# Kernel optimization log

Measured on AMD Instinct MI355X. Metric: run time of the kernel, lower is better.

The kernel has to match this reference:

```python
import jax, jax.numpy as jnp
import numpy as np

N, G, D, H, B = 32768, 1024, 512, 768, 4   # nodes, graphs, hidden, shared, branches
GHD, NHD = 64, 3                           # graph head dim, node head dim (var_output=1)

def setup_inputs() -> dict:
    key = jax.random.key(0)
    ks = jax.random.split(key, 8)
    scale = 0.02
    x = jax.random.normal(ks[0], (N, D), dtype=jnp.float32)
    batch = jnp.sort(jax.random.randint(ks[1], (N,), 0, G, dtype=jnp.int32))
    dataset_name = jax.random.randint(ks[2], (G,), 0, B, dtype=jnp.int32)
    return {
        "x": x,
        "batch": batch,
        "dataset_name": dataset_name,
        "Wg_shared": jax.random.normal(ks[3], (B, D, H), jnp.float32) * scale,
        "bg_shared": jnp.zeros((B, H), jnp.float32),
        "Wg_head": jax.random.normal(ks[4], (B, H, 2 * GHD), jnp.float32) * scale,
        "bg_head": jnp.zeros((B, 2 * GHD), jnp.float32),
        "Wn1": jax.random.normal(ks[5], (B, D, D), jnp.float32) * scale,
        "bn1": jnp.zeros((B, D), jnp.float32),
        "Wn2": jax.random.normal(ks[6], (B, D, 2 * NHD), jnp.float32) * scale,
        "bn2": jnp.zeros((B, 2 * NHD), jnp.float32),
    }

def _select_branch(y, branch_ids):
    # y: [n, B, f], branch_ids: [n] -> [n, f]
    return jnp.take_along_axis(y, branch_ids[:, None, None], axis=1)[:, 0]

def reference(x, batch, dataset_name, Wg_shared, bg_shared, Wg_head, bg_head,
              Wn1, bn1, Wn2, bn2):
    nG = dataset_name.shape[0]
    # --- graph mean pooling (graph_pool_fn with reduction='mean') ---
    counts = jax.ops.segment_sum(jnp.ones((x.shape[0], 1), x.dtype), batch,
                                 num_segments=nG)
    x_graph = jax.ops.segment_sum(x, batch, num_segments=nG) / jnp.maximum(counts, 1.0)
    # --- graph head: per-dataset-ID branch dispatch (dense-MoE form) ---
    hg = jax.nn.relu(jnp.einsum('gd,bdh->gbh', x_graph, Wg_shared) + bg_shared)  # [G,B,H]
    hg_sel = _select_branch(hg, dataset_name)                                    # [G,H]
    og = jnp.einsum('gh,bho->gbo', hg_sel, Wg_head) + bg_head                    # [G,B,2*GHD]
    og_sel = _select_branch(og, dataset_name)
    graph_head = og_sel[:, :GHD]
    graph_var = og_sel[:, GHD:] ** 2
    # --- node head: route nodes by their graph's dataset ID (repeat_interleave) ---
    node_branch = dataset_name[batch]                                            # [N]
    hn = jax.nn.relu(jnp.einsum('nd,bdh->nbh', x, Wn1) + bn1)                    # [N,B,D]
    hn_sel = _select_branch(hn, node_branch)                                     # [N,D]
    on = jnp.einsum('nh,bho->nbo', hn_sel, Wn2) + bn2                            # [N,B,2*NHD]
    on_sel = _select_branch(on, node_branch)
    node_head = on_sel[:, :NHD]
    node_var = on_sel[:, NHD:] ** 2
    # torch returns (outputs, outputs_var); flattened here as 4 arrays
    return (graph_head, node_head, graph_var, node_var)
```

## Files before the change

### kernel.cpp

```cpp
#include <hip/hip_runtime.h>

#define N_NODES 32768
#define G_GRAPHS 1024
#define D_DIM 512
#define H_DIM 768
#define B_BR 4
#define GHD 64
#define NHD 3

#define NH_OFF (G_GRAPHS * GHD)
#define GV_OFF (G_GRAPHS * GHD + N_NODES * NHD)
#define NV_OFF (2 * G_GRAPHS * GHD + N_NODES * NHD)

typedef unsigned short ushort_t;
typedef __attribute__((ext_vector_type(8))) short short8;
typedef __attribute__((ext_vector_type(4))) float f32x4;
typedef __attribute__((ext_vector_type(4))) ushort_t ushort4_t;

__device__ __forceinline__ ushort_t rne_bf16(float v) {
  unsigned bits = __float_as_uint(v);
  return (ushort_t)((bits + 0x7fffu + ((bits >> 16) & 1u)) >> 16);
}

__global__ __launch_bounds__(1024) void segscan_kernel(
    const int* __restrict__ batch, const int* __restrict__ dsname,
    int* __restrict__ gstart, int* __restrict__ goff, int* __restrict__ glist,
    int* __restrict__ cnt, int* __restrict__ gcnt, int* __restrict__ pbase) {
  __shared__ int sg[G_GRAPHS + 1];
  __shared__ int scnt[4], sgcnt[4];
  const int tid = threadIdx.x;
  {
    int g = tid;
    int lo = 0, hi = N_NODES;
    while (lo < hi) { int mid = (lo + hi) >> 1; if (batch[mid] < g) lo = mid + 1; else hi = mid; }
    sg[g] = lo; gstart[g] = lo;
    if (tid == 0) { sg[G_GRAPHS] = N_NODES; gstart[G_GRAPHS] = N_NODES; }
  }
  __syncthreads();
  if (tid < 256) {
    const int lane = tid & 63;
    const int b = tid >> 6;
    int run_n = 0, run_g = 0;
    for (int c = 0; c < G_GRAPHS / 64; ++c) {
      int g = c * 64 + lane;
      int mine = (dsname[g] == b) ? 1 : 0;
      int len = mine ? (sg[g + 1] - sg[g]) : 0;
      int sl = len, so = mine;
#pragma unroll
      for (int off = 1; off < 64; off <<= 1) {
        int tl = __shfl_up(sl, off);
        int to = __shfl_up(so, off);
        if (lane >= off) { sl += tl; so += to; }
      }
      if (mine) {
        goff[g] = run_n + sl - len;
        glist[b * G_GRAPHS + run_g + so - 1] = g;
      }
      run_n += __shfl(sl, 63);
      run_g += __shfl(so, 63);
    }
    if (lane == 0) { scnt[b] = run_n; sgcnt[b] = run_g; }
  }
  __syncthreads();
  if (tid == 0) {
    int p = 0;
    for (int b2 = 0; b2 < 4; ++b2) {
      cnt[b2] = scnt[b2];
      gcnt[b2] = sgcnt[b2];
      pbase[b2] = p;
      p += (scnt[b2] + 63) & ~63;
    }
  }
}

__global__ __launch_bounds__(256) void prep_kernel(
    const float* __restrict__ x, const int* __restrict__ batch,
    const int* __restrict__ dsname, const int* __restrict__ gstart,
    const int* __restrict__ goff,
    int* __restrict__ lists,
    ushort_t* __restrict__ xgb,
    const float* __restrict__ Wn1, ushort_t* __restrict__ WPh,
    const float* __restrict__ Wg1, ushort_t* __restrict__ WG1,
    const float* __restrict__ Wgh, ushort_t* __restrict__ WG2,
    const float* __restrict__ Wn2, ushort_t* __restrict__ W2T) {
  __shared__ float Ws[64][65];
  const int bid = blockIdx.x;
  const int tid = threadIdx.x;

  if (bid < 1024) {
    const int rl = tid >> 6;
    const int cs = tid & 63;
    const int g = bid;
    const int start = gstart[g];
    const int len = gstart[g + 1] - start;
    const int b = dsname[g];
    const int og = goff[g];
    for (int i = tid; i < len; i += 256) lists[b * N_NODES + og + i] = start + i;
    float s0 = 0.f, s1 = 0.f, s2 = 0.f, s3 = 0.f;
    float s4 = 0.f, s5 = 0.f, s6 = 0.f, s7 = 0.f;
    for (int i = rl; i < len; i += 4) {
      const float* sp = x + (size_t)(start + i) * D_DIM + cs * 8;
      float4 v0 = *reinterpret_cast<const float4*>(sp);
      float4 v1 = *reinterpret_cast<const float4*>(sp + 4);
      s0 += v0.x; s1 += v0.y; s2 += v0.z; s3 += v0.w;
      s4 += v1.x; s5 += v1.y; s6 += v1.z; s7 += v1.w;
    }
    float* red = (float*)Ws;
    float* rr = red + (rl * 64 + cs) * 8;
    rr[0] = s0; rr[1] = s1; rr[2] = s2; rr[3] = s3;
    rr[4] = s4; rr[5] = s5; rr[6] = s6; rr[7] = s7;
    __syncthreads();
    if (rl == 0) {
      float inv = (len > 0) ? 1.0f / (float)len : 0.0f;
      short8 h;
#pragma unroll
      for (int k = 0; k < 8; ++k) {
        float tot = red[(0 * 64 + cs) * 8 + k] + red[(1 * 64 + cs) * 8 + k] +
                    red[(2 * 64 + cs) * 8 + k] + red[(3 * 64 + cs) * 8 + k];
        h[k] = (short)rne_bf16(tot * inv);
      }
      *reinterpret_cast<short8*>(xgb + (size_t)g * D_DIM + cs * 8) = h;
    }
  } else {
    const int cid = bid - 1024;
    if (cid < 256) {
      int b = cid >> 6, t = cid & 63;
      int kt = t >> 3, nt = t & 7;
      const float* W = Wn1 + (size_t)b * D_DIM * D_DIM;
      for (int i = tid; i < 64 * 64; i += 256) {
        int k = i >> 6, n = i & 63;
        Ws[k][n] = W[(size_t)(kt * 64 + k) * D_DIM + nt * 64 + n];
      }
      __syncthreads();
      for (int i = tid; i < 64 * 8; i += 256) {
        int n = i >> 3, kq8 = i & 7;
        short8 sh;
#pragma unroll
        for (int j = 0; j < 8; ++j) sh[j] = (short)rne_bf16(Ws[kq8 * 8 + j][n]);
        int gn = nt * 64 + n, gk0 = kt * 64 + kq8 * 8;
        int n16 = gn >> 4, l15 = gn & 15;
        int ks = gk0 >> 5, lq = (gk0 >> 3) & 3;
        size_t off = ((((size_t)b * 32 + n16) * 16 + ks) * 64 + lq * 16 + l15) * 8;
        *reinterpret_cast<short8*>(WPh + off) = sh;
      }
    } else if (cid < 640) {
      int l2 = cid - 256;
      int b = l2 / 96, t = l2 % 96;
      int kt = t / 12, nt = t % 12;
      const float* W = Wg1 + (size_t)b * D_DIM * H_DIM;
      for (int i = tid; i < 64 * 64; i += 256) {
        int k = i >> 6, n = i & 63;
        Ws[k][n] = W[(size_t)(kt * 64 + k) * H_DIM + nt * 64 + n];
      }
      __syncthreads();
      for (int i = tid; i < 64 * 8; i += 256) {
        int n = i >> 3, kq8 = i & 7;
        short8 sh;
#pragma unroll
        for (int j = 0; j < 8; ++j) sh[j] = (short)rne_bf16(Ws[kq8 * 8 + j][n]);
        int gn = nt * 64 + n, gk0 = kt * 64 + kq8 * 8;
        int n16 = gn >> 4, l15 = gn & 15;
        int ks = gk0 >> 5, lq = (gk0 >> 3) & 3;
        size_t off = ((((size_t)b * 48 + n16) * 16 + ks) * 64 + lq * 16 + l15) * 8;
        *reinterpret_cast<short8*>(WG1 + off) = sh;
      }
    } else if (cid < 644) {
      int b = cid - 640;
      const float* W = Wgh + (size_t)b * H_DIM * 2 * GHD;
      for (int i = tid; i < 8 * 24 * 64; i += 256) {
        int n16 = i / (24 * 64);
        int rem = i % (24 * 64);
        int ks = rem / 64, lane = rem % 64;
        int l15 = lane & 15, lq = lane >> 4;
        int o = n16 * 16 + l15;
        short8 sv;
#pragma unroll
        for (int j = 0; j < 8; ++j) {
          int k = ks * 32 + lq * 8 + j;
          sv[j] = (short)rne_bf16(W[(size_t)k * 128 + o]);
        }
        *reinterpret_cast<short8*>(WG2 + (size_t)i * 8 + (size_t)b * (8 * 24 * 64 * 8)) = sv;
      }
    } else {
      int b = cid - 644;
      for (int i = tid; i < 16 * D_DIM; i += 256) {
        int o = i & 15, c = i >> 4;
        float v = (o < 6) ? Wn2[(size_t)b * D_DIM * 6 + c * 6 + o] : 0.0f;
        W2T[(size_t)b * 16 * D_DIM + o * D_DIM + c] = rne_bf16(v);
      }
    }
  }
}

#define NBM 64
#define GRAPH_BLOCKS 128
#define NODE_BLOCKS 576

__global__ __launch_bounds__(512, 2) void mega_kernel(
    const float* __restrict__ x,
    const ushort_t* __restrict__ WPh,
    const float* __restrict__ bn1,
    const ushort_t* __restrict__ W2T, const float* __restrict__ bn2,
    const int* __restrict__ cnt, const int* __restrict__ pbase,
    const int* __restrict__ lists,
    const ushort_t* __restrict__ xgb,
    const ushort_t* __restrict__ WG1, const float* __restrict__ bg_shared,
    const ushort_t* __restrict__ WG2, const float* __restrict__ bg_head,
    const int* __restrict__ gcnt, const int* __restrict__ glist,
    float* __restrict__ out) {
  __shared__ __align__(16) char smem[131072];
  __shared__ int idxbuf[64];

  const int bid = blockIdx.x;
  const int tid = threadIdx.x;
  const int lane = tid & 63;
  const int w = tid >> 6;
  const int l15 = lane & 15;
  const int lq = lane >> 4;

  if (bid >= GRAPH_BLOCKS) {
    const int nb = bid - GRAPH_BLOCKS;
    const int b = (nb & 7) >> 1;
    const int tile = ((nb >> 3) << 1) | (nb & 1);
    const int count = cnt[b];
    const int base = tile * NBM;
    if (base >= count) return;

    ushort_t* Ah = (ushort_t*)smem;
    if (tid < NBM) {
      int r = base + tid;
      idxbuf[tid] = (r < count) ? lists[b * N_NODES + r] : lists[b * N_NODES];
    }
    __syncthreads();

#pragma unroll
    for (int it = 0; it < 8; ++it) {
      int u = it * 512 + tid;
      int r = u >> 6, cp = u & 63;
      const float* sp = x + (size_t)idxbuf[r] * D_DIM + cp * 8;
      float4 v0 = *reinterpret_cast<const float4*>(sp);
      float4 v1 = *reinterpret_cast<const float4*>(sp + 4);
      short8 h;
      h[0] = (short)rne_bf16(v0.x); h[1] = (short)rne_bf16(v0.y);
      h[2] = (short)rne_bf16(v0.z); h[3] = (short)rne_bf16(v0.w);
      h[4] = (short)rne_bf16(v1.x); h[5] = (short)rne_bf16(v1.y);
      h[6] = (short)rne_bf16(v1.z); h[7] = (short)rne_bf16(v1.w);
      *reinterpret_cast<short8*>((char*)Ah + r * 1024 + ((cp ^ (r & 7)) << 4)) = h;
    }
    __syncthreads();

    const ushort_t* __restrict__ wph =
        WPh + (((size_t)b * 32 + w * 4) * 16) * 512 + (size_t)lane * 8;
    ushort_t* Bl = (ushort_t*)(smem + 65536 + w * 8192);

#pragma unroll
    for (int ct = 0; ct < 4; ++ct) {
      __builtin_amdgcn_global_load_lds(
          (const __attribute__((address_space(1))) void*)(wph + (size_t)(ct * 16) * 512),
          (__attribute__((address_space(3))) void*)(Bl + ct * 512),
          16, 0, 0);
    }

    f32x4 acc[4][4];
#pragma unroll
    for (int i = 0; i < 4; ++i)
#pragma unroll
      for (int j = 0; j < 4; ++j) acc[i][j] = (f32x4){0.f, 0.f, 0.f, 0.f};

#pragma unroll
    for (int ks = 0; ks < 16; ++ks) {
      const int nks = (ks + 1) & 15;
      ushort_t* Bnx = Bl + ((ks + 1) & 1) * 2048;
#pragma unroll
      for (int ct = 0; ct < 4; ++ct) {
        __builtin_amdgcn_global_load_lds(
            (const __attribute__((address_space(1))) void*)(wph + (size_t)(ct * 16 + nks) * 512),
            (__attribute__((address_space(3))) void*)(Bnx + ct * 512),
            16, 0, 0);
      }
      asm volatile("s_waitcnt vmcnt(4)" ::: "memory");
      __builtin_amdgcn_sched_barrier(0);
      const ushort_t* Bc = Bl + (ks & 1) * 2048;
      short8 ah[4], bh[4];
#pragma unroll
      for (int rt = 0; rt < 4; ++rt) {
        int R = rt * 16 + l15;
        int byteoff = R * 1024 + ((ks * 64 + lq * 16) ^ ((R & 7) << 4));
        ah[rt] = *reinterpret_cast<const short8*>((const char*)Ah + byteoff);
      }
#pragma unroll
      for (int ct = 0; ct < 4; ++ct)
        bh[ct] = *reinterpret_cast<const short8*>(Bc + ct * 512 + lane * 8);
#pragma unroll
      for (int ct = 0; ct < 4; ++ct) {
#pragma unroll
        for (int rt = 0; rt < 4; ++rt) {
          acc[rt][ct] = __builtin_amdgcn_mfma_f32_16x16x32_bf16(ah[rt], bh[ct], acc[rt][ct], 0, 0, 0);
        }
      }
    }

    __syncthreads();
    ushort_t* hn = Ah;
#pragma unroll
    for (int ct = 0; ct < 4; ++ct) {
      int n = w * 64 + ct * 16 + l15;
      float bias = bn1[b * D_DIM + n];
#pragma unroll
      for (int rt = 0; rt < 4; ++rt) {
#pragma unroll
        for (int j = 0; j < 4; ++j) {
          int row = rt * 16 + lq * 4 + j;
          float v = fmaxf(acc[rt][ct][j] + bias, 0.0f);
          int byteoff = row * 1024 + ((n * 2) ^ ((row & 7) << 4));
          *reinterpret_cast<ushort_t*>((char*)hn + byteoff) = rne_bf16(v);
        }
      }
    }
    __syncthreads();

    if (w < 4) {
      f32x4 acc2 = (f32x4){0.f, 0.f, 0.f, 0.f};
      const ushort_t* __restrict__ w2 =
          W2T + (size_t)b * (16 * 512) + (size_t)l15 * 512 + lq * 8;
      const int R = w * 16 + l15;
#pragma unroll
      for (int ks = 0; ks < 16; ++ks) {
        int byteoff = R * 1024 + ((ks * 64 + lq * 16) ^ ((R & 7) << 4));
        short8 a2 = *reinterpret_cast<const short8*>((const char*)hn + byteoff);
        short8 b2 = *reinterpret_cast<const short8*>(w2 + ks * 32);
        acc2 = __builtin_amdgcn_mfma_f32_16x16x32_bf16(a2, b2, acc2, 0, 0, 0);
      }
      int o = l15;
      if (o < 6) {
        float bo = bn2[b * 6 + o];
#pragma unroll
        for (int j = 0; j < 4; ++j) {
          int r = w * 16 + lq * 4 + j;
          if (base + r < count) {
            int n = idxbuf[r];
            float v = acc2[j] + bo;
            if (o < NHD) out[NH_OFF + n * NHD + o] = v;
            else out[NV_OFF + n * NHD + (o - NHD)] = v * v;
          }
        }
      }
    }
  } else {
    const int gb = bid;
    const int b = (gb & 7) >> 1;
    const int tile = ((gb >> 3) << 1) | (gb & 1);
    const int gc = gcnt[b];
    const int base = tile * 32;
    if (base >= gc) return;

    ushort_t* Ag = (ushort_t*)smem;
    if (tid < 32) {
      int r = base + tid;
      idxbuf[tid] = (r < gc) ? glist[b * G_GRAPHS + r] : glist[b * G_GRAPHS];
    }
    __syncthreads();

#pragma unroll
    for (int it = 0; it < 4; ++it) {
      int u = it * 512 + tid;
      int r = u >> 6, cp = u & 63;
      const ushort_t* sp = xgb + (size_t)idxbuf[r] * D_DIM + cp * 8;
      short8 h = *reinterpret_cast<const short8*>(sp);
      int byteoff = r * 1024 + ((cp * 16) ^ ((r & 7) << 4));
      *reinterpret_cast<short8*>((char*)Ag + byteoff) = h;
    }
    __syncthreads();

    f32x4 acc[2][6];
#pragma unroll
    for (int i = 0; i < 2; ++i)
#pragma unroll
      for (int j = 0; j < 6; ++j) acc[i][j] = (f32x4){0.f, 0.f, 0.f, 0.f};

    const ushort_t* __restrict__ g1 =
        WG1 + (((size_t)b * 48 + w * 6) * 16) * 512 + (size_t)lane * 8;

    for (int ks = 0; ks < 16; ++ks) {
      short8 ah[2];
#pragma unroll
      for (int rt = 0; rt < 2; ++rt) {
        int R = rt * 16 + l15;
        int byteoff = R * 1024 + ((ks * 64 + lq * 16) ^ ((R & 7) << 4));
        ah[rt] = *reinterpret_cast<const short8*>((const char*)Ag + byteoff);
      }
#pragma unroll
      for (int ct = 0; ct < 6; ++ct) {
        short8 bh = *reinterpret_cast<const short8*>(g1 + (size_t)(ct * 16 + ks) * 512);
#pragma unroll
        for (int rt = 0; rt < 2; ++rt) {
          acc[rt][ct] = __builtin_amdgcn_mfma_f32_16x16x32_bf16(ah[rt], bh, acc[rt][ct], 0, 0, 0);
        }
      }
    }

    __syncthreads();
    ushort_t* hgs = (ushort_t*)smem;
#pragma unroll
    for (int ct = 0; ct < 6; ++ct) {
      int n = w * 96 + ct * 16 + l15;
      float bias = bg_shared[b * H_DIM + n];
#pragma unroll
      for (int rt = 0; rt < 2; ++rt) {
#pragma unroll
        for (int j = 0; j < 4; ++j) {
          int row = rt * 16 + lq * 4 + j;
          float v = fmaxf(acc[rt][ct][j] + bias, 0.0f);
          int byteoff = row * 1536 + ((n * 2) ^ ((row & 7) << 4));
          *reinterpret_cast<ushort_t*>((char*)hgs + byteoff) = rne_bf16(v);
        }
      }
    }
    __syncthreads();

    f32x4 acc2[2];
    acc2[0] = (f32x4){0.f, 0.f, 0.f, 0.f};
    acc2[1] = (f32x4){0.f, 0.f, 0.f, 0.f};
    const ushort_t* __restrict__ g2 =
        WG2 + ((size_t)(b * 8 + w) * 24 * 64 + lane) * 8;

    for (int ks = 0; ks < 24; ++ks) {
      short8 b2 = *reinterpret_cast<const short8*>(g2 + (size_t)ks * 512);
#pragma unroll
      for (int rt = 0; rt < 2; ++rt) {
        int R = rt * 16 + l15;
        int byteoff = R * 1536 + ((ks * 64 + lq * 16) ^ ((R & 7) << 4));
        short8 a2 = *reinterpret_cast<const short8*>((const char*)hgs + byteoff);
        acc2[rt] = __builtin_amdgcn_mfma_f32_16x16x32_bf16(a2, b2, acc2[rt], 0, 0, 0);
      }
    }

    int o = w * 16 + l15;
    float bo = bg_head[b * 2 * GHD + o];
#pragma unroll
    for (int rt = 0; rt < 2; ++rt) {
#pragma unroll
      for (int j = 0; j < 4; ++j) {
        int r = rt * 16 + lq * 4 + j;
        if (base + r < gc) {
          int g = idxbuf[r];
          float v = acc2[rt][j] + bo;
          if (o < GHD) out[g * GHD + o] = v;
          else out[GV_OFF + g * GHD + (o - GHD)] = v * v;
        }
      }
    }
  }
}

extern "C" void kernel_launch(void* const* d_in, const int* in_sizes, int n_in,
                              void* d_out, int out_size, void* d_ws, size_t ws_size,
                              hipStream_t stream) {
  const float* x         = (const float*)d_in[0];
  const int*   batch     = (const int*)d_in[1];
  const int*   dsname    = (const int*)d_in[2];
  const float* Wg_shared = (const float*)d_in[3];
  const float* bg_shared = (const float*)d_in[4];
  const float* Wg_head   = (const float*)d_in[5];
  const float* bg_head   = (const float*)d_in[6];
  const float* Wn1       = (const float*)d_in[7];
  const float* bn1       = (const float*)d_in[8];
  const float* Wn2       = (const float*)d_in[9];
  const float* bn2       = (const float*)d_in[10];
  float* out = (float*)d_out;

  int* ws_i   = (int*)d_ws;
  int* cnt    = ws_i;
  int* gcnt   = ws_i + 8;
  int* pbase  = ws_i + 12;
  int* gstart = ws_i + 16;
  int* goff   = ws_i + 1056;
  int* glist  = ws_i + 2080;
  int* lists  = ws_i + 6176;
  ushort_t* xgb  = (ushort_t*)(ws_i + 137248);
  ushort_t* WPh  = xgb + 524288;
  ushort_t* W2T  = WPh + 1048576;
  ushort_t* WG1  = W2T + 32768;
  ushort_t* WG2  = WG1 + 1572864;

  segscan_kernel<<<1, 1024, 0, stream>>>(batch, dsname, gstart, goff, glist,
                                         cnt, gcnt, pbase);
  prep_kernel<<<1672, 256, 0, stream>>>(x, batch, dsname, gstart, goff,
                                        lists, xgb,
                                        Wn1, WPh, Wg_shared, WG1,
                                        Wg_head, WG2, Wn2, W2T);
  mega_kernel<<<GRAPH_BLOCKS + NODE_BLOCKS, 512, 0, stream>>>(
      x, WPh, bn1, W2T, bn2, cnt, pbase, lists,
      xgb, WG1, bg_shared, WG2, bg_head, gcnt, glist, out);
}
```

Before: 89.40 us.

## Fuse graph mean pooling into graph GEMM blocks of mega kernel

```diff
diff --git a/kernel.cpp b/kernel.cpp
--- a/kernel.cpp
+++ b/kernel.cpp
@@ -74,11 +74,8 @@
 }
 
 __global__ __launch_bounds__(256) void prep_kernel(
-    const float* __restrict__ x, const int* __restrict__ batch,
-    const int* __restrict__ dsname, const int* __restrict__ gstart,
-    const int* __restrict__ goff,
-    int* __restrict__ lists,
-    ushort_t* __restrict__ xgb,
+    const int* __restrict__ gstart, const int* __restrict__ goff,
+    const int* __restrict__ dsname, int* __restrict__ lists,
     const float* __restrict__ Wn1, ushort_t* __restrict__ WPh,
     const float* __restrict__ Wg1, ushort_t* __restrict__ WG1,
     const float* __restrict__ Wgh, ushort_t* __restrict__ WG2,
@@ -87,107 +84,81 @@
   const int bid = blockIdx.x;
   const int tid = threadIdx.x;
 
-  if (bid < 1024) {
-    const int rl = tid >> 6;
-    const int cs = tid & 63;
-    const int g = bid;
-    const int start = gstart[g];
-    const int len = gstart[g + 1] - start;
-    const int b = dsname[g];
-    const int og = goff[g];
-    for (int i = tid; i < len; i += 256) lists[b * N_NODES + og + i] = start + i;
-    float s0 = 0.f, s1 = 0.f, s2 = 0.f, s3 = 0.f;
-    float s4 = 0.f, s5 = 0.f, s6 = 0.f, s7 = 0.f;
-    for (int i = rl; i < len; i += 4) {
-      const float* sp = x + (size_t)(start + i) * D_DIM + cs * 8;
-      float4 v0 = *reinterpret_cast<const float4*>(sp);
-      float4 v1 = *reinterpret_cast<const float4*>(sp + 4);
-      s0 += v0.x; s1 += v0.y; s2 += v0.z; s3 += v0.w;
-      s4 += v1.x; s5 += v1.y; s6 += v1.z; s7 += v1.w;
-    }
-    float* red = (float*)Ws;
-    float* rr = red + (rl * 64 + cs) * 8;
-    rr[0] = s0; rr[1] = s1; rr[2] = s2; rr[3] = s3;
-    rr[4] = s4; rr[5] = s5; rr[6] = s6; rr[7] = s7;
-    __syncthreads();
-    if (rl == 0) {
-      float inv = (len > 0) ? 1.0f / (float)len : 0.0f;
-      short8 h;
-#pragma unroll
-      for (int k = 0; k < 8; ++k) {
-        float tot = red[(0 * 64 + cs) * 8 + k] + red[(1 * 64 + cs) * 8 + k] +
-                    red[(2 * 64 + cs) * 8 + k] + red[(3 * 64 + cs) * 8 + k];
-        h[k] = (short)rne_bf16(tot * inv);
-      }
-      *reinterpret_cast<short8*>(xgb + (size_t)g * D_DIM + cs * 8) = h;
+  if (bid < 256) {
+    int b = bid >> 6, t = bid & 63;
+    int kt = t >> 3, nt = t & 7;
+    const float* W = Wn1 + (size_t)b * D_DIM * D_DIM;
+    for (int i = tid; i < 64 * 64; i += 256) {
+      int k = i >> 6, n = i & 63;
+      Ws[k][n] = W[(size_t)(kt * 64 + k) * D_DIM + nt * 64 + n];
+    }
+    __syncthreads();
+    for (int i = tid; i < 64 * 8; i += 256) {
+      int n = i >> 3, kq8 = i & 7;
+      short8 sh;
+#pragma unroll
+      for (int j = 0; j < 8; ++j) sh[j] = (short)rne_bf16(Ws[kq8 * 8 + j][n]);
+      int gn = nt * 64 + n, gk0 = kt * 64 + kq8 * 8;
+      int n16 = gn >> 4, l15 = gn & 15;
+      int ks = gk0 >> 5, lq = (gk0 >> 3) & 3;
+      size_t off = ((((size_t)b * 32 + n16) * 16 + ks) * 64 + lq * 16 + l15) * 8;
+      *reinterpret_cast<short8*>(WPh + off) = sh;
+    }
+  } else if (bid < 640) {
+    int l2 = bid - 256;
+    int b = l2 / 96, t = l2 % 96;
+    int kt = t / 12, nt = t % 12;
+    const float* W = Wg1 + (size_t)b * D_DIM * H_DIM;
+    for (int i = tid; i < 64 * 64; i += 256) {
+      int k = i >> 6, n = i & 63;
+      Ws[k][n] = W[(size_t)(kt * 64 + k) * H_DIM + nt * 64 + n];
+    }
+    __syncthreads();
+    for (int i = tid; i < 64 * 8; i += 256) {
+      int n = i >> 3, kq8 = i & 7;
+      short8 sh;
+#pragma unroll
+      for (int j = 0; j < 8; ++j) sh[j] = (short)rne_bf16(Ws[kq8 * 8 + j][n]);
+      int gn = nt * 64 + n, gk0 = kt * 64 + kq8 * 8;
+      int n16 = gn >> 4, l15 = gn & 15;
+      int ks = gk0 >> 5, lq = (gk0 >> 3) & 3;
+      size_t off = ((((size_t)b * 48 + n16) * 16 + ks) * 64 + lq * 16 + l15) * 8;
+      *reinterpret_cast<short8*>(WG1 + off) = sh;
+    }
+  } else if (bid < 644) {
+    int b = bid - 640;
+    const float* W = Wgh + (size_t)b * H_DIM * 2 * GHD;
+    for (int i = tid; i < 8 * 24 * 64; i += 256) {
+      int n16 = i / (24 * 64);
+      int rem = i % (24 * 64);
+      int ks = rem / 64, lane = rem % 64;
+      int l15 = lane & 15, lq = lane >> 4;
+      int o = n16 * 16 + l15;
+      short8 sv;
+#pragma unroll
+      for (int j = 0; j < 8; ++j) {
+        int k = ks * 32 + lq * 8 + j;
+        sv[j] = (short)rne_bf16(W[(size_t)k * 128 + o]);
+      }
+      *reinterpret_cast<short8*>(WG2 + (size_t)i * 8 + (size_t)b * (8 * 24 * 64 * 8)) = sv;
+    }
+  } else if (bid < 648) {
+    int b = bid - 644;
+    for (int i = tid; i < 16 * D_DIM; i += 256) {
+      int o = i & 15, c = i >> 4;
+      float v = (o < 6) ? Wn2[(size_t)b * D_DIM * 6 + c * 6 + o] : 0.0f;
+      W2T[(size_t)b * 16 * D_DIM + o * D_DIM + c] = rne_bf16(v);
     }
   } else {
-    const int cid = bid - 1024;
-    if (cid < 256) {
-      int b = cid >> 6, t = cid & 63;
-      int kt = t >> 3, nt = t & 7;
-      const float* W = Wn1 + (size_t)b * D_DIM * D_DIM;
-      for (int i = tid; i < 64 * 64; i += 256) {
-        int k = i >> 6, n = i & 63;
-        Ws[k][n] = W[(size_t)(kt * 64 + k) * D_DIM + nt * 64 + n];
-      }
-      __syncthreads();
-      for (int i = tid; i < 64 * 8; i += 256) {
-        int n = i >> 3, kq8 = i & 7;
-        short8 sh;
-#pragma unroll
-        for (int j = 0; j < 8; ++j) sh[j] = (short)rne_bf16(Ws[kq8 * 8 + j][n]);
-        int gn = nt * 64 + n, gk0 = kt * 64 + kq8 * 8;
-        int n16 = gn >> 4, l15 = gn & 15;
-        int ks = gk0 >> 5, lq = (gk0 >> 3) & 3;
-        size_t off = ((((size_t)b * 32 + n16) * 16 + ks) * 64 + lq * 16 + l15) * 8;
-        *reinterpret_cast<short8*>(WPh + off) = sh;
-      }
-    } else if (cid < 640) {
-      int l2 = cid - 256;
-      int b = l2 / 96, t = l2 % 96;
-      int kt = t / 12, nt = t % 12;
-      const float* W = Wg1 + (size_t)b * D_DIM * H_DIM;
-      for (int i = tid; i < 64 * 64; i += 256) {
-        int k = i >> 6, n = i & 63;
-        Ws[k][n] = W[(size_t)(kt * 64 + k) * H_DIM + nt * 64 + n];
-      }
-      __syncthreads();
-      for (int i = tid; i < 64 * 8; i += 256) {
-        int n = i >> 3, kq8 = i & 7;
-        short8 sh;
-#pragma unroll
-        for (int j = 0; j < 8; ++j) sh[j] = (short)rne_bf16(Ws[kq8 * 8 + j][n]);
-        int gn = nt * 64 + n, gk0 = kt * 64 + kq8 * 8;
-        int n16 = gn >> 4, l15 = gn & 15;
-        int ks = gk0 >> 5, lq = (gk0 >> 3) & 3;
-        size_t off = ((((size_t)b * 48 + n16) * 16 + ks) * 64 + lq * 16 + l15) * 8;
-        *reinterpret_cast<short8*>(WG1 + off) = sh;
-      }
-    } else if (cid < 644) {
-      int b = cid - 640;
-      const float* W = Wgh + (size_t)b * H_DIM * 2 * GHD;
-      for (int i = tid; i < 8 * 24 * 64; i += 256) {
-        int n16 = i / (24 * 64);
-        int rem = i % (24 * 64);
-        int ks = rem / 64, lane = rem % 64;
-        int l15 = lane & 15, lq = lane >> 4;
-        int o = n16 * 16 + l15;
-        short8 sv;
-#pragma unroll
-        for (int j = 0; j < 8; ++j) {
-          int k = ks * 32 + lq * 8 + j;
-          sv[j] = (short)rne_bf16(W[(size_t)k * 128 + o]);
-        }
-        *reinterpret_cast<short8*>(WG2 + (size_t)i * 8 + (size_t)b * (8 * 24 * 64 * 8)) = sv;
-      }
-    } else {
-      int b = cid - 644;
-      for (int i = tid; i < 16 * D_DIM; i += 256) {
-        int o = i & 15, c = i >> 4;
-        float v = (o < 6) ? Wn2[(size_t)b * D_DIM * 6 + c * 6 + o] : 0.0f;
-        W2T[(size_t)b * 16 * D_DIM + o * D_DIM + c] = rne_bf16(v);
-      }
+    int blk = bid - 648;
+#pragma unroll
+    for (int j = 0; j < 8; ++j) {
+      int g = blk * 8 + j;
+      int start = gstart[g];
+      int len = gstart[g + 1] - start;
+      int b = dsname[g];
+      int og = goff[g];
+      for (int i = tid; i < len; i += 256) lists[b * N_NODES + og + i] = start + i;
     }
   }
 }
@@ -202,8 +173,7 @@
     const float* __restrict__ bn1,
     const ushort_t* __restrict__ W2T, const float* __restrict__ bn2,
     const int* __restrict__ cnt, const int* __restrict__ pbase,
-    const int* __restrict__ lists,
-    const ushort_t* __restrict__ xgb,
+    const int* __restrict__ lists, const int* __restrict__ gstart,
     const ushort_t* __restrict__ WG1, const float* __restrict__ bg_shared,
     const ushort_t* __restrict__ WG2, const float* __restrict__ bg_head,
     const int* __restrict__ gcnt, const int* __restrict__ glist,
@@ -361,14 +331,32 @@
     }
     __syncthreads();
 
-#pragma unroll
-    for (int it = 0; it < 4; ++it) {
-      int u = it * 512 + tid;
-      int r = u >> 6, cp = u & 63;
-      const ushort_t* sp = xgb + (size_t)idxbuf[r] * D_DIM + cp * 8;
-      short8 h = *reinterpret_cast<const short8*>(sp);
-      int byteoff = r * 1024 + ((cp * 16) ^ ((r & 7) << 4));
-      *reinterpret_cast<short8*>((char*)Ag + byteoff) = h;
+    {
+      const int gi = tid >> 4;
+      const int sub = tid & 15;
+      int g = idxbuf[gi];
+      int start = gstart[g], end = gstart[g + 1];
+      float s[32];
+#pragma unroll
+      for (int k = 0; k < 32; ++k) s[k] = 0.f;
+      const float* bp = x + (size_t)start * D_DIM + sub * 32;
+      for (int i = 0; i < end - start; ++i) {
+#pragma unroll
+        for (int q = 0; q < 8; ++q) {
+          float4 v = *reinterpret_cast<const float4*>(bp + (size_t)i * D_DIM + q * 4);
+          s[q * 4 + 0] += v.x; s[q * 4 + 1] += v.y;
+          s[q * 4 + 2] += v.z; s[q * 4 + 3] += v.w;
+        }
+      }
+      float inv = (end > start) ? 1.0f / (float)(end - start) : 0.0f;
+#pragma unroll
+      for (int qq = 0; qq < 4; ++qq) {
+        short8 h;
+#pragma unroll
+        for (int k = 0; k < 8; ++k) h[k] = (short)rne_bf16(s[qq * 8 + k] * inv);
+        int cp = sub * 4 + qq;
+        *reinterpret_cast<short8*>((char*)Ag + gi * 1024 + ((cp << 4) ^ ((gi & 7) << 4))) = h;
+      }
     }
     __syncthreads();
 
@@ -477,19 +465,17 @@
   int* goff   = ws_i + 1056;
   int* glist  = ws_i + 2080;
   int* lists  = ws_i + 6176;
-  ushort_t* xgb  = (ushort_t*)(ws_i + 137248);
-  ushort_t* WPh  = xgb + 524288;
+  ushort_t* WPh  = (ushort_t*)(ws_i + 137248);
   ushort_t* W2T  = WPh + 1048576;
   ushort_t* WG1  = W2T + 32768;
   ushort_t* WG2  = WG1 + 1572864;
 
   segscan_kernel<<<1, 1024, 0, stream>>>(batch, dsname, gstart, goff, glist,
                                          cnt, gcnt, pbase);
-  prep_kernel<<<1672, 256, 0, stream>>>(x, batch, dsname, gstart, goff,
-                                        lists, xgb,
-                                        Wn1, WPh, Wg_shared, WG1,
-                                        Wg_head, WG2, Wn2, W2T);
+  prep_kernel<<<776, 256, 0, stream>>>(gstart, goff, dsname, lists,
+                                       Wn1, WPh, Wg_shared, WG1,
+                                       Wg_head, WG2, Wn2, W2T);
   mega_kernel<<<GRAPH_BLOCKS + NODE_BLOCKS, 512, 0, stream>>>(
-      x, WPh, bn1, W2T, bn2, cnt, pbase, lists,
-      xgb, WG1, bg_shared, WG2, bg_head, gcnt, glist, out);
+      x, WPh, bn1, W2T, bn2, cnt, pbase, lists, gstart,
+      WG1, bg_shared, WG2, bg_head, gcnt, glist, out);
 }
```

Result: slower. 119.8 us (+34.1%).

## Move graph mean pooling into mega kernel with flag-synchronized graph blocks

Applied to the files above, without the earlier changes.

```diff
diff --git a/kernel.cpp b/kernel.cpp
--- a/kernel.cpp
+++ b/kernel.cpp
@@ -74,11 +74,8 @@
 }
 
 __global__ __launch_bounds__(256) void prep_kernel(
-    const float* __restrict__ x, const int* __restrict__ batch,
-    const int* __restrict__ dsname, const int* __restrict__ gstart,
-    const int* __restrict__ goff,
-    int* __restrict__ lists,
-    ushort_t* __restrict__ xgb,
+    const int* __restrict__ gstart, const int* __restrict__ goff,
+    const int* __restrict__ dsname, int* __restrict__ lists,
     const float* __restrict__ Wn1, ushort_t* __restrict__ WPh,
     const float* __restrict__ Wg1, ushort_t* __restrict__ WG1,
     const float* __restrict__ Wgh, ushort_t* __restrict__ WG2,
@@ -87,114 +84,89 @@
   const int bid = blockIdx.x;
   const int tid = threadIdx.x;
 
-  if (bid < 1024) {
-    const int rl = tid >> 6;
-    const int cs = tid & 63;
-    const int g = bid;
-    const int start = gstart[g];
-    const int len = gstart[g + 1] - start;
-    const int b = dsname[g];
-    const int og = goff[g];
-    for (int i = tid; i < len; i += 256) lists[b * N_NODES + og + i] = start + i;
-    float s0 = 0.f, s1 = 0.f, s2 = 0.f, s3 = 0.f;
-    float s4 = 0.f, s5 = 0.f, s6 = 0.f, s7 = 0.f;
-    for (int i = rl; i < len; i += 4) {
-      const float* sp = x + (size_t)(start + i) * D_DIM + cs * 8;
-      float4 v0 = *reinterpret_cast<const float4*>(sp);
-      float4 v1 = *reinterpret_cast<const float4*>(sp + 4);
-      s0 += v0.x; s1 += v0.y; s2 += v0.z; s3 += v0.w;
-      s4 += v1.x; s5 += v1.y; s6 += v1.z; s7 += v1.w;
-    }
-    float* red = (float*)Ws;
-    float* rr = red + (rl * 64 + cs) * 8;
-    rr[0] = s0; rr[1] = s1; rr[2] = s2; rr[3] = s3;
-    rr[4] = s4; rr[5] = s5; rr[6] = s6; rr[7] = s7;
-    __syncthreads();
-    if (rl == 0) {
-      float inv = (len > 0) ? 1.0f / (float)len : 0.0f;
-      short8 h;
-#pragma unroll
-      for (int k = 0; k < 8; ++k) {
-        float tot = red[(0 * 64 + cs) * 8 + k] + red[(1 * 64 + cs) * 8 + k] +
-                    red[(2 * 64 + cs) * 8 + k] + red[(3 * 64 + cs) * 8 + k];
-        h[k] = (short)rne_bf16(tot * inv);
-      }
-      *reinterpret_cast<short8*>(xgb + (size_t)g * D_DIM + cs * 8) = h;
+  if (bid < 256) {
+    int b = bid >> 6, t = bid & 63;
+    int kt = t >> 3, nt = t & 7;
+    const float* W = Wn1 + (size_t)b * D_DIM * D_DIM;
+    for (int i = tid; i < 64 * 64; i += 256) {
+      int k = i >> 6, n = i & 63;
+      Ws[k][n] = W[(size_t)(kt * 64 + k) * D_DIM + nt * 64 + n];
+    }
+    __syncthreads();
+    for (int i = tid; i < 64 * 8; i += 256) {
+      int n = i >> 3, kq8 = i & 7;
+      short8 sh;
+#pragma unroll
+      for (int j = 0; j < 8; ++j) sh[j] = (short)rne_bf16(Ws[kq8 * 8 + j][n]);
+      int gn = nt * 64 + n, gk0 = kt * 64 + kq8 * 8;
+      int n16 = gn >> 4, l15 = gn & 15;
+      int ks = gk0 >> 5, lq = (gk0 >> 3) & 3;
+      size_t off = ((((size_t)b * 32 + n16) * 16 + ks) * 64 + lq * 16 + l15) * 8;
+      *reinterpret_cast<short8*>(WPh + off) = sh;
+    }
+  } else if (bid < 640) {
+    int l2 = bid - 256;
+    int b = l2 / 96, t = l2 % 96;
+    int kt = t / 12, nt = t % 12;
+    const float* W = Wg1 + (size_t)b * D_DIM * H_DIM;
+    for (int i = tid; i < 64 * 64; i += 256) {
+      int k = i >> 6, n = i & 63;
+      Ws[k][n] = W[(size_t)(kt * 64 + k) * H_DIM + nt * 64 + n];
+    }
+    __syncthreads();
+    for (int i = tid; i < 64 * 8; i += 256) {
+      int n = i >> 3, kq8 = i & 7;
+      short8 sh;
+#pragma unroll
+      for (int j = 0; j < 8; ++j) sh[j] = (short)rne_bf16(Ws[kq8 * 8 + j][n]);
+      int gn = nt * 64 + n, gk0 = kt * 64 + kq8 * 8;
+      int n16 = gn >> 4, l15 = gn & 15;
+      int ks = gk0 >> 5, lq = (gk0 >> 3) & 3;
+      size_t off = ((((size_t)b * 48 + n16) * 16 + ks) * 64 + lq * 16 + l15) * 8;
+      *reinterpret_cast<short8*>(WG1 + off) = sh;
+    }
+  } else if (bid < 644) {
+    int b = bid - 640;
+    const float* W = Wgh + (size_t)b * H_DIM * 2 * GHD;
+    for (int i = tid; i < 8 * 24 * 64; i += 256) {
+      int n16 = i / (24 * 64);
+      int rem = i % (24 * 64);
+      int ks = rem / 64, lane = rem % 64;
+      int l15 = lane & 15, lq = lane >> 4;
+      int o = n16 * 16 + l15;
+      short8 sv;
+#pragma unroll
+      for (int j = 0; j < 8; ++j) {
+        int k = ks * 32 + lq * 8 + j;
+        sv[j] = (short)rne_bf16(W[(size_t)k * 128 + o]);
+      }
+      *reinterpret_cast<short8*>(WG2 + (size_t)i * 8 + (size_t)b * (8 * 24 * 64 * 8)) = sv;
+    }
+  } else if (bid < 648) {
+    int b = bid - 644;
+    for (int i = tid; i < 16 * D_DIM; i += 256) {
+      int o = i & 15, c = i >> 4;
+      float v = (o < 6) ? Wn2[(size_t)b * D_DIM * 6 + c * 6 + o] : 0.0f;
+      W2T[(size_t)b * 16 * D_DIM + o * D_DIM + c] = rne_bf16(v);
     }
   } else {
-    const int cid = bid - 1024;
-    if (cid < 256) {
-      int b = cid >> 6, t = cid & 63;
-      int kt = t >> 3, nt = t & 7;
-      const float* W = Wn1 + (size_t)b * D_DIM * D_DIM;
-      for (int i = tid; i < 64 * 64; i += 256) {
-        int k = i >> 6, n = i & 63;
-        Ws[k][n] = W[(size_t)(kt * 64 + k) * D_DIM + nt * 64 + n];
-      }
-      __syncthreads();
-      for (int i = tid; i < 64 * 8; i += 256) {
-        int n = i >> 3, kq8 = i & 7;
-        short8 sh;
-#pragma unroll
-        for (int j = 0; j < 8; ++j) sh[j] = (short)rne_bf16(Ws[kq8 * 8 + j][n]);
-        int gn = nt * 64 + n, gk0 = kt * 64 + kq8 * 8;
-        int n16 = gn >> 4, l15 = gn & 15;
-        int ks = gk0 >> 5, lq = (gk0 >> 3) & 3;
-        size_t off = ((((size_t)b * 32 + n16) * 16 + ks) * 64 + lq * 16 + l15) * 8;
-        *reinterpret_cast<short8*>(WPh + off) = sh;
-      }
-    } else if (cid < 640) {
-      int l2 = cid - 256;
-      int b = l2 / 96, t = l2 % 96;
-      int kt = t / 12, nt = t % 12;
-      const float* W = Wg1 + (size_t)b * D_DIM * H_DIM;
-      for (int i = tid; i < 64 * 64; i += 256) {
-        int k = i >> 6, n = i & 63;
-        Ws[k][n] = W[(size_t)(kt * 64 + k) * H_DIM + nt * 64 + n];
-      }
-      __syncthreads();
-      for (int i = tid; i < 64 * 8; i += 256) {
-        int n = i >> 3, kq8 = i & 7;
-        short8 sh;
-#pragma unroll
-        for (int j = 0; j < 8; ++j) sh[j] = (short)rne_bf16(Ws[kq8 * 8 + j][n]);
-        int gn = nt * 64 + n, gk0 = kt * 64 + kq8 * 8;
-        int n16 = gn >> 4, l15 = gn & 15;
-        int ks = gk0 >> 5, lq = (gk0 >> 3) & 3;
-        size_t off = ((((size_t)b * 48 + n16) * 16 + ks) * 64 + lq * 16 + l15) * 8;
-        *reinterpret_cast<short8*>(WG1 + off) = sh;
-      }
-    } else if (cid < 644) {
-      int b = cid - 640;
-      const float* W = Wgh + (size_t)b * H_DIM * 2 * GHD;
-      for (int i = tid; i < 8 * 24 * 64; i += 256) {
-        int n16 = i / (24 * 64);
-        int rem = i % (24 * 64);
-        int ks = rem / 64, lane = rem % 64;
-        int l15 = lane & 15, lq = lane >> 4;
-        int o = n16 * 16 + l15;
-        short8 sv;
-#pragma unroll
-        for (int j = 0; j < 8; ++j) {
-          int k = ks * 32 + lq * 8 + j;
-          sv[j] = (short)rne_bf16(W[(size_t)k * 128 + o]);
-        }
-        *reinterpret_cast<short8*>(WG2 + (size_t)i * 8 + (size_t)b * (8 * 24 * 64 * 8)) = sv;
-      }
-    } else {
-      int b = cid - 644;
-      for (int i = tid; i < 16 * D_DIM; i += 256) {
-        int o = i & 15, c = i >> 4;
-        float v = (o < 6) ? Wn2[(size_t)b * D_DIM * 6 + c * 6 + o] : 0.0f;
-        W2T[(size_t)b * 16 * D_DIM + o * D_DIM + c] = rne_bf16(v);
-      }
+    int blk = bid - 648;
+#pragma unroll
+    for (int j = 0; j < 8; ++j) {
+      int g = blk * 8 + j;
+      int start = gstart[g];
+      int len = gstart[g + 1] - start;
+      int b = dsname[g];
+      int og = goff[g];
+      for (int i = tid; i < len; i += 256) lists[b * N_NODES + og + i] = start + i;
     }
   }
 }
 
 #define NBM 64
+#define POOL_BLOCKS 1024
+#define NODE_BLOCKS 576
 #define GRAPH_BLOCKS 128
-#define NODE_BLOCKS 576
 
 __global__ __launch_bounds__(512, 2) void mega_kernel(
     const float* __restrict__ x,
@@ -202,8 +174,8 @@
     const float* __restrict__ bn1,
     const ushort_t* __restrict__ W2T, const float* __restrict__ bn2,
     const int* __restrict__ cnt, const int* __restrict__ pbase,
-    const int* __restrict__ lists,
-    const ushort_t* __restrict__ xgb,
+    const int* __restrict__ lists, const int* __restrict__ gstart,
+    ushort_t* __restrict__ xgb, int* __restrict__ poolflag,
     const ushort_t* __restrict__ WG1, const float* __restrict__ bg_shared,
     const ushort_t* __restrict__ WG2, const float* __restrict__ bg_head,
     const int* __restrict__ gcnt, const int* __restrict__ glist,
@@ -218,8 +190,44 @@
   const int l15 = lane & 15;
   const int lq = lane >> 4;
 
-  if (bid >= GRAPH_BLOCKS) {
-    const int nb = bid - GRAPH_BLOCKS;
+  if (bid < POOL_BLOCKS) {
+    const int rl = tid >> 6;
+    const int cs = tid & 63;
+    const int g = bid;
+    const int start = gstart[g];
+    const int len = gstart[g + 1] - start;
+    float s0 = 0.f, s1 = 0.f, s2 = 0.f, s3 = 0.f;
+    float s4 = 0.f, s5 = 0.f, s6 = 0.f, s7 = 0.f;
+    for (int i = rl; i < len; i += 8) {
+      const float* sp = x + (size_t)(start + i) * D_DIM + cs * 8;
+      float4 v0 = *reinterpret_cast<const float4*>(sp);
+      float4 v1 = *reinterpret_cast<const float4*>(sp + 4);
+      s0 += v0.x; s1 += v0.y; s2 += v0.z; s3 += v0.w;
+      s4 += v1.x; s5 += v1.y; s6 += v1.z; s7 += v1.w;
+    }
+    float* red = (float*)smem;
+    float* rr = red + (rl * 64 + cs) * 8;
+    rr[0] = s0; rr[1] = s1; rr[2] = s2; rr[3] = s3;
+    rr[4] = s4; rr[5] = s5; rr[6] = s6; rr[7] = s7;
+    __syncthreads();
+    if (rl == 0) {
+      float inv = (len > 0) ? 1.0f / (float)len : 0.0f;
+      short8 h;
+#pragma unroll
+      for (int k = 0; k < 8; ++k) {
+        float tot = 0.f;
+#pragma unroll
+        for (int p = 0; p < 8; ++p) tot += red[(p * 64 + cs) * 8 + k];
+        h[k] = (short)rne_bf16(tot * inv);
+      }
+      *reinterpret_cast<short8*>(xgb + (size_t)g * D_DIM + cs * 8) = h;
+    }
+    __threadfence();
+    __syncthreads();
+    if (tid == 0)
+      __hip_atomic_fetch_add(poolflag, 1, __ATOMIC_RELEASE, __HIP_MEMORY_SCOPE_AGENT);
+  } else if (bid < POOL_BLOCKS + NODE_BLOCKS) {
+    const int nb = bid - POOL_BLOCKS;
     const int b = (nb & 7) >> 1;
     const int tile = ((nb >> 3) << 1) | (nb & 1);
     const int count = cnt[b];
@@ -347,12 +355,18 @@
       }
     }
   } else {
-    const int gb = bid;
+    const int gb = bid - POOL_BLOCKS - NODE_BLOCKS;
     const int b = (gb & 7) >> 1;
     const int tile = ((gb >> 3) << 1) | (gb & 1);
     const int gc = gcnt[b];
     const int base = tile * 32;
     if (base >= gc) return;
+
+    if (tid == 0) {
+      while (__hip_atomic_load(poolflag, __ATOMIC_ACQUIRE,
+                               __HIP_MEMORY_SCOPE_AGENT) < G_GRAPHS) {}
+    }
+    __syncthreads();
 
     ushort_t* Ag = (ushort_t*)smem;
     if (tid < 32) {
@@ -474,6 +488,7 @@
   int* gcnt   = ws_i + 8;
   int* pbase  = ws_i + 12;
   int* gstart = ws_i + 16;
+  int* poolflag = ws_i + 1044;
   int* goff   = ws_i + 1056;
   int* glist  = ws_i + 2080;
   int* lists  = ws_i + 6176;
@@ -483,13 +498,13 @@
   ushort_t* WG1  = W2T + 32768;
   ushort_t* WG2  = WG1 + 1572864;
 
+  hipMemsetAsync(poolflag, 0, sizeof(int), stream);
   segscan_kernel<<<1, 1024, 0, stream>>>(batch, dsname, gstart, goff, glist,
                                          cnt, gcnt, pbase);
-  prep_kernel<<<1672, 256, 0, stream>>>(x, batch, dsname, gstart, goff,
-                                        lists, xgb,
-                                        Wn1, WPh, Wg_shared, WG1,
-                                        Wg_head, WG2, Wn2, W2T);
-  mega_kernel<<<GRAPH_BLOCKS + NODE_BLOCKS, 512, 0, stream>>>(
-      x, WPh, bn1, W2T, bn2, cnt, pbase, lists,
-      xgb, WG1, bg_shared, WG2, bg_head, gcnt, glist, out);
+  prep_kernel<<<776, 256, 0, stream>>>(gstart, goff, dsname, lists,
+                                       Wn1, WPh, Wg_shared, WG1,
+                                       Wg_head, WG2, Wn2, W2T);
+  mega_kernel<<<POOL_BLOCKS + NODE_BLOCKS + GRAPH_BLOCKS, 512, 0, stream>>>(
+      x, WPh, bn1, W2T, bn2, cnt, pbase, lists, gstart,
+      xgb, poolflag, WG1, bg_shared, WG2, bg_head, gcnt, glist, out);
 }
```

Result: slower. 262.5 us (+193.6%).
